# Kernel tuning notes

Hardware: AMD Instinct MI355X
Metric: run time of the kernel (lower is better)

The kernel has to match this reference:

```python
import jax, jax.numpy as jnp
import numpy as np

# Minifloat meta: fp8 e4m3-style (4 exponent bits, 3 mantissa bits, bias = 2^(E-1)-1)
EXP_BITS = 4
MAN_BITS = 3


def quantize_minifloat(t, exp_bits=EXP_BITS, man_bits=MAN_BITS):
    """Fake-quantize a float tensor to a minifloat grid (round-to-nearest, saturate).

    Simulates extract_minifloat_component + dequantize: snap each value to the
    nearest representable minifloat with `exp_bits` exponent bits and
    `man_bits` mantissa bits (IEEE-style bias, subnormals supported via the
    clamped minimum exponent, saturating clamp at max normal value).
    """
    bias = 2 ** (exp_bits - 1) - 1
    emin = 1 - bias                      # min normal exponent
    emax = bias                          # max exponent (no inf/nan specials)
    max_val = (2.0 - 2.0 ** (-man_bits)) * (2.0 ** emax)
    ax = jnp.abs(t)
    # exponent of each value; zeros are safe because 0/scale == 0
    e = jnp.floor(jnp.log2(jnp.where(ax > 0, ax, 1.0)))
    e = jnp.maximum(e, float(emin))      # flush into subnormal grid
    scale = jnp.exp2(e - man_bits)       # quantization step at this exponent
    q = jnp.round(t / scale) * scale
    return jnp.clip(q, -max_val, max_val)


def setup_inputs() -> dict:
    key = jax.random.key(0)
    k1, k2, k3 = jax.random.split(key, 3)
    tokens, d_in, d_out = 32768, 1024, 1024
    x = jax.random.normal(k1, (tokens, d_in), dtype=jnp.float32)
    w = jax.random.normal(k2, (d_out, d_in), dtype=jnp.float32) * 0.02
    b = jax.random.normal(k3, (d_out,), dtype=jnp.float32) * 0.02
    return {"x": x, "w": w, "b": b}


def reference(x, w, b):
    # layer_type 'XqWqBq': minifloat-quantize activations, weight and bias,
    # then fused linear: y = xq @ wq.T + bq   (nn.Linear convention, w: [out, in])
    xq = quantize_minifloat(x)
    wq = quantize_minifloat(w)
    bq = quantize_minifloat(b)
    return jnp.einsum("ti,oi->to", xq, wq) + bq
```

## Files before the change

kernel.cpp:

```cpp
#include <hip/hip_runtime.h>

typedef float f32x4 __attribute__((ext_vector_type(4)));
typedef long  i64x2 __attribute__((ext_vector_type(2)));

__device__ __forceinline__ float quant1(float t) {
    unsigned bits = __float_as_uint(t);
    int eb = (int)((bits & 0x7fffffffu) >> 23);
    eb = eb < 121 ? 121 : eb;
    float m = __uint_as_float((unsigned)(257 - eb) << 23);
    float s = __uint_as_float((unsigned)(eb - 3) << 23);
    float q = rintf(t * m) * s;
    q = fminf(q, 240.0f);
    q = fmaxf(q, -240.0f);
    return q;
}

__device__ __forceinline__ unsigned fp8enc(float t) {
    unsigned b  = __float_as_uint(t);
    unsigned sg = (b >> 24) & 0x80u;
    unsigned a  = b & 0x7fffffffu;
    unsigned mag;
    if (a < 0x3C800000u) {
        mag = (unsigned)(int)rintf(__uint_as_float(a) * 512.0f);
    } else {
        mag = ((a + 0x7FFFFu + ((a >> 20) & 1u)) >> 20) - 0x3C0u;
        mag = mag > 0x77u ? 0x77u : mag;
    }
    return sg | mag;
}

__global__ void quant_tile_fp8_kernel(const float* __restrict__ x, const float* __restrict__ w,
                                      unsigned char* __restrict__ xq, unsigned char* __restrict__ wq,
                                      long long nAc, long long nTot, int K, int ktlog) {
    const long long stride = (long long)gridDim.x * blockDim.x;
    const int nktm1 = (1 << ktlog) - 1;
    for (long long chunk = (long long)blockIdx.x * blockDim.x + threadIdx.x;
         chunk < nTot; chunk += stride) {
        const bool isA = chunk < nAc;
        const float* src = isA ? x : w;
        unsigned char* dst = isA ? xq : wq;
        const long long cc = isA ? chunk : chunk - nAc;
        const long long tile = cc >> 9;
        const int c = (int)(cc & 511);
        const int r = c >> 2, kgpos = c & 3;
        const int kg = kgpos ^ ((r >> 1) & 3);
        const long long blk = tile >> ktlog;
        const int kt0 = (int)(tile & nktm1);
        const float* s0 = src + (blk * 128 + r) * (long long)K + kt0 * 64 + kg * 8;
        float4 a0 = *(const float4*)(s0);
        float4 a1 = *(const float4*)(s0 + 4);
        float4 b0 = *(const float4*)(s0 + 32);
        float4 b1 = *(const float4*)(s0 + 36);
        uint4 o;
        o.x = fp8enc(a0.x) | (fp8enc(a0.y) << 8) | (fp8enc(a0.z) << 16) | (fp8enc(a0.w) << 24);
        o.y = fp8enc(a1.x) | (fp8enc(a1.y) << 8) | (fp8enc(a1.z) << 16) | (fp8enc(a1.w) << 24);
        o.z = fp8enc(b0.x) | (fp8enc(b0.y) << 8) | (fp8enc(b0.z) << 16) | (fp8enc(b0.w) << 24);
        o.w = fp8enc(b1.x) | (fp8enc(b1.y) << 8) | (fp8enc(b1.z) << 16) | (fp8enc(b1.w) << 24);
        ((uint4*)dst)[cc] = o;
    }
}

#define BM 128
#define BN 128
#define BKB 64

__device__ __forceinline__ void gload_lds16(const void* g, void* l) {
    __builtin_amdgcn_global_load_lds(
        (const __attribute__((address_space(1))) void*)g,
        (__attribute__((address_space(3))) void*)l, 16, 0, 0);
}

__global__ __launch_bounds__(256, 2) void gemm_fp8t_kernel(
    const unsigned char* __restrict__ At,
    const unsigned char* __restrict__ Bt,
    const float* __restrict__ bias,
    float* __restrict__ C, int M, int N, int K)
{
    __shared__ __align__(16) unsigned char As[BM * BKB];
    __shared__ __align__(16) unsigned char Bs[BN * BKB];

    const int t    = threadIdx.x;
    const int lane = t & 63;
    const int wid  = t >> 6;
    const int wm   = (wid >> 1) * 64;
    const int wn   = (wid & 1) * 64;
    const int fr   = lane & 15;
    const int kg   = lane >> 4;

    const int nkt = K / BKB;
    const unsigned char* pA = At + (size_t)blockIdx.x * nkt * 8192;
    const unsigned char* pB = Bt + (size_t)blockIdx.y * nkt * 8192;

    int offA[4], offB[4];
    #pragma unroll
    for (int m = 0; m < 4; ++m) {
        int row = wm + m * 16 + fr;
        offA[m] = row * 64 + ((kg ^ ((row >> 1) & 3)) << 4);
    }
    #pragma unroll
    for (int n = 0; n < 4; ++n) {
        int row = wn + n * 16 + fr;
        offB[n] = row * 64 + ((kg ^ ((row >> 1) & 3)) << 4);
    }

    f32x4 acc[4][4] = {};

    for (int kt = 0; kt < nkt; ++kt) {
        gload_lds16(pA + t * 16,        &As[t * 16]);
        gload_lds16(pA + t * 16 + 4096, &As[t * 16 + 4096]);
        gload_lds16(pB + t * 16,        &Bs[t * 16]);
        gload_lds16(pB + t * 16 + 4096, &Bs[t * 16 + 4096]);
        pA += 8192; pB += 8192;
        __syncthreads();

        i64x2 av[4], bv[4];
        #pragma unroll
        for (int m = 0; m < 4; ++m) av[m] = *(const i64x2*)&As[offA[m]];
        #pragma unroll
        for (int n = 0; n < 4; ++n) bv[n] = *(const i64x2*)&Bs[offB[n]];

        #pragma unroll
        for (int m = 0; m < 4; ++m)
            #pragma unroll
            for (int n = 0; n < 4; ++n) {
                acc[m][n] = __builtin_amdgcn_mfma_f32_16x16x32_fp8_fp8(
                    av[m][0], bv[n][0], acc[m][n], 0, 0, 0);
                acc[m][n] = __builtin_amdgcn_mfma_f32_16x16x32_fp8_fp8(
                    av[m][1], bv[n][1], acc[m][n], 0, 0, 0);
            }

        __syncthreads();
    }

    #pragma unroll
    for (int m = 0; m < 4; ++m) {
        int row = blockIdx.x * BM + wm + m * 16 + kg * 4;
        #pragma unroll
        for (int n = 0; n < 4; ++n) {
            int col = blockIdx.y * BN + wn + n * 16 + fr;
            float bb = quant1(bias[col]);
            #pragma unroll
            for (int r = 0; r < 4; ++r)
                C[(size_t)(row + r) * N + col] = acc[m][n][r] + bb;
        }
    }
}

__global__ void naive_gemm_kernel(const float* __restrict__ x, const float* __restrict__ w,
                                  const float* __restrict__ b, float* __restrict__ out,
                                  int M, int N, int K) {
    int col = blockIdx.x * blockDim.x + threadIdx.x;
    int row = blockIdx.y;
    if (col >= N || row >= M) return;
    const float* xr = x + (size_t)row * K;
    const float* wr = w + (size_t)col * K;
    float acc = 0.f;
    for (int k = 0; k < K; ++k) acc += quant1(xr[k]) * quant1(wr[k]);
    out[(size_t)row * N + col] = acc + quant1(b[col]);
}

extern "C" void kernel_launch(void* const* d_in, const int* in_sizes, int n_in,
                              void* d_out, int out_size, void* d_ws, size_t ws_size,
                              hipStream_t stream) {
    const float* x = (const float*)d_in[0];
    const float* w = (const float*)d_in[1];
    const float* b = (const float*)d_in[2];
    float* out = (float*)d_out;

    const int xsz = in_sizes[0];
    const int wsz = in_sizes[1];
    const int N   = in_sizes[2];
    const int K   = wsz / N;
    const int M   = xsz / K;

    const size_t need = (size_t)xsz + (size_t)wsz;
    const int nkt = K / BKB;
    const bool nkt_pow2 = nkt > 0 && (nkt & (nkt - 1)) == 0;

    const bool fast_ok = (ws_size >= need) && nkt_pow2 &&
                         (M % BM == 0) && (N % BN == 0) && (K % BKB == 0);

    if (fast_ok) {
        unsigned char* xq = (unsigned char*)d_ws;
        unsigned char* wq = (unsigned char*)d_ws + xsz;

        int ktlog = 0;
        while ((1 << ktlog) < nkt) ++ktlog;

        const long long nAc = (long long)xsz / 16;
        const long long nTot = nAc + (long long)wsz / 16;
        quant_tile_fp8_kernel<<<2048, 256, 0, stream>>>(x, w, xq, wq, nAc, nTot, K, ktlog);

        dim3 grid(M / BM, N / BN);
        gemm_fp8t_kernel<<<grid, 256, 0, stream>>>(xq, wq, b, out, M, N, K);
    } else {
        dim3 grid((N + 255) / 256, M);
        naive_gemm_kernel<<<grid, 256, 0, stream>>>(x, w, b, out, M, N, K);
    }
}
```

Measured before the change: 284.3 us.

## Switch GEMM to 32x32x64 scaled FP8 MFMA with matching tile layout

Replaces the 16x16x32 FP8 MFMA pairs with the gfx950 scaled 32x32x64 f8f6f4 MFMA, using unit scales. The quantize kernel's LDS chunk layout changes so each lane can read a contiguous 32-byte K slice, and the epilogue is remapped to the 32x32 output layout. An explicit vmcnt wait is added before the barrier. The aim is to cut MFMA instruction count and issue overhead per K tile, with the same LDS traffic. It depends on the scaled-MFMA operand and scale semantics matching the plain FP8 result.

```diff
diff --git a/kernel.cpp b/kernel.cpp
--- a/kernel.cpp
+++ b/kernel.cpp
@@ -1,7 +1,7 @@
 #include <hip/hip_runtime.h>
 
-typedef float f32x4 __attribute__((ext_vector_type(4)));
-typedef long  i64x2 __attribute__((ext_vector_type(2)));
+typedef float f32x16 __attribute__((ext_vector_type(16)));
+typedef int   i32x8  __attribute__((ext_vector_type(8)));
 
 __device__ __forceinline__ float quant1(float t) {
     unsigned bits = __float_as_uint(t);
@@ -42,15 +42,15 @@
         const long long cc = isA ? chunk : chunk - nAc;
         const long long tile = cc >> 9;
         const int c = (int)(cc & 511);
-        const int r = c >> 2, kgpos = c & 3;
-        const int kg = kgpos ^ ((r >> 1) & 3);
+        const int r = c >> 2, p = c & 3;
+        const int s = p ^ ((r >> 1) & 3);
         const long long blk = tile >> ktlog;
         const int kt0 = (int)(tile & nktm1);
-        const float* s0 = src + (blk * 128 + r) * (long long)K + kt0 * 64 + kg * 8;
+        const float* s0 = src + (blk * 128 + r) * (long long)K + kt0 * 64 + s * 16;
         float4 a0 = *(const float4*)(s0);
         float4 a1 = *(const float4*)(s0 + 4);
-        float4 b0 = *(const float4*)(s0 + 32);
-        float4 b1 = *(const float4*)(s0 + 36);
+        float4 b0 = *(const float4*)(s0 + 8);
+        float4 b1 = *(const float4*)(s0 + 12);
         uint4 o;
         o.x = fp8enc(a0.x) | (fp8enc(a0.y) << 8) | (fp8enc(a0.z) << 16) | (fp8enc(a0.w) << 24);
         o.y = fp8enc(a1.x) | (fp8enc(a1.y) << 8) | (fp8enc(a1.z) << 16) | (fp8enc(a1.w) << 24);
@@ -70,7 +70,7 @@
         (__attribute__((address_space(3))) void*)l, 16, 0, 0);
 }
 
-__global__ __launch_bounds__(256, 2) void gemm_fp8t_kernel(
+__global__ __launch_bounds__(256, 2) void gemm_fp8s_kernel(
     const unsigned char* __restrict__ At,
     const unsigned char* __restrict__ Bt,
     const float* __restrict__ bias,
@@ -84,26 +84,26 @@
     const int wid  = t >> 6;
     const int wm   = (wid >> 1) * 64;
     const int wn   = (wid & 1) * 64;
-    const int fr   = lane & 15;
-    const int kg   = lane >> 4;
+    const int l31  = lane & 31;
+    const int hi2  = lane >> 5;
 
     const int nkt = K / BKB;
     const unsigned char* pA = At + (size_t)blockIdx.x * nkt * 8192;
     const unsigned char* pB = Bt + (size_t)blockIdx.y * nkt * 8192;
 
-    int offA[4], offB[4];
+    int offA[2], offB[2];
     #pragma unroll
-    for (int m = 0; m < 4; ++m) {
-        int row = wm + m * 16 + fr;
-        offA[m] = row * 64 + ((kg ^ ((row >> 1) & 3)) << 4);
+    for (int mi = 0; mi < 2; ++mi) {
+        int row = wm + mi * 32 + l31;
+        offA[mi] = row * 64 + ((((hi2 << 1)) ^ ((row >> 1) & 3)) << 4);
     }
     #pragma unroll
-    for (int n = 0; n < 4; ++n) {
-        int row = wn + n * 16 + fr;
-        offB[n] = row * 64 + ((kg ^ ((row >> 1) & 3)) << 4);
-    }
-
-    f32x4 acc[4][4] = {};
+    for (int ni = 0; ni < 2; ++ni) {
+        int row = wn + ni * 32 + l31;
+        offB[ni] = row * 64 + ((((hi2 << 1)) ^ ((row >> 1) & 3)) << 4);
+    }
+
+    f32x16 acc[2][2] = {};
 
     for (int kt = 0; kt < nkt; ++kt) {
         gload_lds16(pA + t * 16,        &As[t * 16]);
@@ -111,37 +111,51 @@
         gload_lds16(pB + t * 16,        &Bs[t * 16]);
         gload_lds16(pB + t * 16 + 4096, &Bs[t * 16 + 4096]);
         pA += 8192; pB += 8192;
+
+        asm volatile("s_waitcnt vmcnt(0)" ::: "memory");
+        __builtin_amdgcn_sched_barrier(0);
         __syncthreads();
 
-        i64x2 av[4], bv[4];
-        #pragma unroll
-        for (int m = 0; m < 4; ++m) av[m] = *(const i64x2*)&As[offA[m]];
-        #pragma unroll
-        for (int n = 0; n < 4; ++n) bv[n] = *(const i64x2*)&Bs[offB[n]];
-
-        #pragma unroll
-        for (int m = 0; m < 4; ++m)
+        i32x8 av[2], bv[2];
+        #pragma unroll
+        for (int mi = 0; mi < 2; ++mi) {
+            uint4 lo = *(const uint4*)&As[offA[mi]];
+            uint4 hi = *(const uint4*)&As[offA[mi] ^ 16];
+            i32x8 v; v[0]=(int)lo.x; v[1]=(int)lo.y; v[2]=(int)lo.z; v[3]=(int)lo.w;
+                     v[4]=(int)hi.x; v[5]=(int)hi.y; v[6]=(int)hi.z; v[7]=(int)hi.w;
+            av[mi] = v;
+        }
+        #pragma unroll
+        for (int ni = 0; ni < 2; ++ni) {
+            uint4 lo = *(const uint4*)&Bs[offB[ni]];
+            uint4 hi = *(const uint4*)&Bs[offB[ni] ^ 16];
+            i32x8 v; v[0]=(int)lo.x; v[1]=(int)lo.y; v[2]=(int)lo.z; v[3]=(int)lo.w;
+                     v[4]=(int)hi.x; v[5]=(int)hi.y; v[6]=(int)hi.z; v[7]=(int)hi.w;
+            bv[ni] = v;
+        }
+
+        #pragma unroll
+        for (int mi = 0; mi < 2; ++mi)
             #pragma unroll
-            for (int n = 0; n < 4; ++n) {
-                acc[m][n] = __builtin_amdgcn_mfma_f32_16x16x32_fp8_fp8(
-                    av[m][0], bv[n][0], acc[m][n], 0, 0, 0);
-                acc[m][n] = __builtin_amdgcn_mfma_f32_16x16x32_fp8_fp8(
-                    av[m][1], bv[n][1], acc[m][n], 0, 0, 0);
-            }
+            for (int ni = 0; ni < 2; ++ni)
+                acc[mi][ni] = __builtin_amdgcn_mfma_scale_f32_32x32x64_f8f6f4(
+                    av[mi], bv[ni], acc[mi][ni], 0, 0, 0, 127, 0, 127);
 
         __syncthreads();
     }
 
     #pragma unroll
-    for (int m = 0; m < 4; ++m) {
-        int row = blockIdx.x * BM + wm + m * 16 + kg * 4;
-        #pragma unroll
-        for (int n = 0; n < 4; ++n) {
-            int col = blockIdx.y * BN + wn + n * 16 + fr;
+    for (int mi = 0; mi < 2; ++mi) {
+        int row0 = blockIdx.x * BM + wm + mi * 32 + hi2 * 4;
+        #pragma unroll
+        for (int ni = 0; ni < 2; ++ni) {
+            int col = blockIdx.y * BN + wn + ni * 32 + l31;
             float bb = quant1(bias[col]);
             #pragma unroll
-            for (int r = 0; r < 4; ++r)
-                C[(size_t)(row + r) * N + col] = acc[m][n][r] + bb;
+            for (int reg = 0; reg < 16; ++reg) {
+                int row = row0 + (reg & 3) + 8 * (reg >> 2);
+                C[(size_t)row * N + col] = acc[mi][ni][reg] + bb;
+            }
         }
     }
 }
@@ -192,7 +206,7 @@
         quant_tile_fp8_kernel<<<2048, 256, 0, stream>>>(x, w, xq, wq, nAc, nTot, K, ktlog);
 
         dim3 grid(M / BM, N / BN);
-        gemm_fp8t_kernel<<<grid, 256, 0, stream>>>(xq, wq, b, out, M, N, K);
+        gemm_fp8s_kernel<<<grid, 256, 0, stream>>>(xq, wq, b, out, M, N, K);
     } else {
         dim3 grid((N + 255) / 256, M);
         naive_gemm_kernel<<<grid, 256, 0, stream>>>(x, w, b, out, M, N, K);
```

Result: no change. 279.3 us (-1.7%).
